# Performance work log

Measured on AMD Instinct MI355X. Metric: run time of the kernel, lower is better.

## Reference

```python
import jax, jax.numpy as jnp
import numpy as np

EPS = 1e-6

def setup_inputs() -> dict:
    key = jax.random.key(0)
    ks = jax.random.split(key, 5)
    B, C, H, W = 16, 512, 64, 64
    D = C // 8
    x = jax.random.normal(ks[0], (B, C, H, W), dtype=jnp.float32)
    Wq = jax.random.normal(ks[1], (D, C), dtype=jnp.float32) * (1.0 / np.sqrt(C))
    Wk = jax.random.normal(ks[2], (D, C), dtype=jnp.float32) * (1.0 / np.sqrt(C))
    Wv = jax.random.normal(ks[3], (C, C), dtype=jnp.float32) * (1.0 / np.sqrt(C))
    bq = jnp.zeros((D,), jnp.float32)
    bk = jnp.zeros((D,), jnp.float32)
    bv = jnp.zeros((C,), jnp.float32)
    gamma = jnp.ones((1,), jnp.float32)
    return {"x": x, "Wq": Wq, "bq": bq, "Wk": Wk, "bk": bk, "Wv": Wv, "bv": bv, "gamma": gamma}

def reference(x, Wq, bq, Wk, bk, Wv, bv, gamma):
    B, C, H, W = x.shape
    n = H * W
    xf = x.reshape(B, C, n)                                   # flatten spatial -> sequence
    # 1x1 convs == per-pixel linear projections
    Q = jnp.einsum('dc,bcn->bnd', Wq, xf) + bq                # (B, n, d)
    K = jnp.einsum('dc,bcn->bdn', Wk, xf) + bk[:, None]       # (B, d, n)
    V = jnp.einsum('dc,bcn->bdn', Wv, xf) + bv[:, None]       # (B, C, n)
    Q = jax.nn.softplus(Q)
    K = jax.nn.softplus(K)
    KV = jnp.einsum('bmn,bcn->bmc', K, V)                     # (B, d, C) linear-attention aggregation
    norm = 1.0 / jnp.einsum('bnm,bm->bn', Q, K.sum(-1) + EPS)  # (B, n)
    wv = jnp.einsum('bnm,bmc,bn->bcn', Q, KV, norm)           # (B, C, n)
    return (x + gamma[0] * wv.reshape(B, C, H, W))
```

## Files before the change

kernel.cpp:

```cpp
#include <hip/hip_runtime.h>
#include <hip/hip_bf16.h>
#include <math.h>

#define BB 16
#define CC 512
#define DD 64
#define NN 4096
#define EPSV 1e-6f
#define NCH 8

typedef __attribute__((ext_vector_type(8))) short short8;
typedef __attribute__((ext_vector_type(4))) short s16x4;
typedef __attribute__((ext_vector_type(4))) float f32x4;

__device__ __forceinline__ float softplus_f(float v) {
    return fmaxf(v, 0.0f) + __logf(1.0f + __expf(-fabsf(v)));
}
__device__ __forceinline__ short bf16s(float f) {
    __hip_bfloat16 h = __float2bfloat16(f);
    return __builtin_bit_cast(short, h);
}
__device__ __forceinline__ float sbf16(short s) {
    return __bfloat162float(__builtin_bit_cast(__hip_bfloat16, s));
}

__global__ __launch_bounds__(256) void k_prep(const float* __restrict__ Wq,
                                              const float* __restrict__ Wk,
                                              __hip_bfloat16* __restrict__ Wcat,
                                              float* __restrict__ Ksum) {
    int blk = blockIdx.x;
    if (blk < 256) {
        int i = blk * 256 + threadIdx.x;
        int j = i >> 9, c = i & 511;
        float v = (j < DD) ? Wq[j * CC + c] : Wk[(j - DD) * CC + c];
        Wcat[i] = __float2bfloat16(v);
    } else {
        f32x4 z = {0.f, 0.f, 0.f, 0.f};
        reinterpret_cast<f32x4*>(Ksum)[threadIdx.x] = z;
    }
}

__global__ __launch_bounds__(256) void k_proj(const float* __restrict__ x,
                                              const __hip_bfloat16* __restrict__ Wcat,
                                              const float* __restrict__ bq,
                                              const float* __restrict__ bk,
                                              __hip_bfloat16* __restrict__ Qb,
                                              __hip_bfloat16* __restrict__ Kb,
                                              __hip_bfloat16* __restrict__ xb16,
                                              float* __restrict__ Ksum) {
    __shared__ unsigned short xs[2][32][132];
    __shared__ unsigned short ws[2][128][40];

    int b = blockIdx.y;
    int n_blk = blockIdx.x * 128;
    int t = threadIdx.x;
    int wave = t >> 6, lane = t & 63;
    int nwl = wave * 32;
    int n_wave = n_blk + nwl;
    int l16 = lane & 15, g = lane >> 4;

    int sv = t & 31;
    int sc = t >> 5;
    int wj = t >> 1;
    int wh = t & 1;

    const float* xb = x + (size_t)b * CC * NN + n_blk + sv * 4;
    unsigned short* xg = reinterpret_cast<unsigned short*>(xb16)
                         + (size_t)b * CC * NN + n_blk + sv * 4;
    const unsigned short* wg = reinterpret_cast<const unsigned short*>(Wcat)
                               + (size_t)wj * 512 + wh * 16;

    f32x4 xr[4];
    s16x4 wr[4];

    auto loadx = [&](int c0) {
#pragma unroll
        for (int i = 0; i < 4; ++i)
            xr[i] = *reinterpret_cast<const f32x4*>(xb + (size_t)(c0 + sc + i * 8) * NN);
    };
    auto loadw = [&](int c0) {
#pragma unroll
        for (int k = 0; k < 4; ++k)
            wr[k] = *reinterpret_cast<const s16x4*>(wg + c0 + k * 4);
    };
    auto writex = [&](int bi, int c0) {
#pragma unroll
        for (int i = 0; i < 4; ++i) {
            s16x4 pv;
#pragma unroll
            for (int j = 0; j < 4; ++j) pv[j] = bf16s(xr[i][j]);
            *reinterpret_cast<s16x4*>(&xs[bi][sc + i * 8][sv * 4]) = pv;
            *reinterpret_cast<s16x4*>(&xg[(size_t)(c0 + sc + i * 8) * NN]) = pv;
        }
    };
    auto writew = [&](int bi) {
#pragma unroll
        for (int k = 0; k < 4; ++k)
            *reinterpret_cast<s16x4*>(&ws[bi][wj][wh * 16 + k * 4]) = wr[k];
    };

    f32x4 accQ[2][4] = {};
    f32x4 accK[4][2] = {};

    loadx(0); loadw(0);
    writex(0, 0); writew(0);

    for (int ck = 0; ck < 16; ++ck) {
        int cur = ck & 1;
        if (ck < 15) { loadx((ck + 1) * 32); loadw((ck + 1) * 32); }
        asm volatile("s_waitcnt lgkmcnt(0)" ::: "memory");
        __builtin_amdgcn_s_barrier();
        short8 xf[2], wf[8];
#pragma unroll
        for (int nf = 0; nf < 2; ++nf) {
            short8 v;
#pragma unroll
            for (int e = 0; e < 8; ++e)
                v[e] = (short)xs[cur][g * 8 + e][nwl + nf * 16 + l16];
            xf[nf] = v;
        }
#pragma unroll
        for (int jf = 0; jf < 8; ++jf)
            wf[jf] = *reinterpret_cast<const short8*>(&ws[cur][jf * 16 + l16][g * 8]);
#pragma unroll
        for (int nf = 0; nf < 2; ++nf)
#pragma unroll
            for (int jf = 0; jf < 4; ++jf)
                accQ[nf][jf] = __builtin_amdgcn_mfma_f32_16x16x32_bf16(xf[nf], wf[jf], accQ[nf][jf], 0, 0, 0);
#pragma unroll
        for (int jf = 0; jf < 4; ++jf)
#pragma unroll
            for (int nf = 0; nf < 2; ++nf)
                accK[jf][nf] = __builtin_amdgcn_mfma_f32_16x16x32_bf16(wf[4 + jf], xf[nf], accK[jf][nf], 0, 0, 0);
        if (ck < 15) { writex(cur ^ 1, (ck + 1) * 32); writew(cur ^ 1); }
    }

#pragma unroll
    for (int nf = 0; nf < 2; ++nf)
#pragma unroll
        for (int jf = 0; jf < 4; ++jf)
#pragma unroll
            for (int r = 0; r < 4; ++r) {
                int n = n_wave + nf * 16 + 4 * g + r;
                int j = jf * 16 + l16;
                float v = softplus_f(accQ[nf][jf][r] + bq[j]);
                Qb[((size_t)b * NN + n) * DD + j] = __float2bfloat16(v);
            }
#pragma unroll
    for (int jf = 0; jf < 4; ++jf)
#pragma unroll
        for (int r = 0; r < 4; ++r) {
            int m = jf * 16 + 4 * g + r;
            float s = 0.f;
#pragma unroll
            for (int nf = 0; nf < 2; ++nf) {
                int n = n_wave + nf * 16 + l16;
                float v = softplus_f(accK[jf][nf][r] + bk[m]);
                Kb[((size_t)b * DD + m) * NN + n] = __float2bfloat16(v);
                s += v;
            }
            s += __shfl_xor(s, 1, 64);
            s += __shfl_xor(s, 2, 64);
            s += __shfl_xor(s, 4, 64);
            s += __shfl_xor(s, 8, 64);
            if (l16 == 0) atomicAdd(&Ksum[b * DD + m], s);
        }
}

__global__ __launch_bounds__(256) void k_kx(const __hip_bfloat16* __restrict__ Kb,
                                            const __hip_bfloat16* __restrict__ xb16,
                                            float* __restrict__ KXp) {
    int b = blockIdx.z;
    int ch = blockIdx.y;
    int n0 = ch * 512;
    int c0 = blockIdx.x * 256;
    int wave = threadIdx.x >> 6, lane = threadIdx.x & 63;
    int cw = c0 + wave * 64;
    int l16 = lane & 15, g = lane >> 4;

    f32x4 acc[4][4] = {};
    const __hip_bfloat16* kp = Kb + (size_t)b * DD * NN;
    const __hip_bfloat16* xp = xb16 + (size_t)b * CC * NN;

#pragma unroll 4
    for (int ks = 0; ks < 16; ++ks) {
        int nk = n0 + ks * 32 + g * 8;
        short8 af[4], bf[4];
#pragma unroll
        for (int mi = 0; mi < 4; ++mi)
            af[mi] = *reinterpret_cast<const short8*>(kp + (size_t)(mi * 16 + l16) * NN + nk);
#pragma unroll
        for (int cj = 0; cj < 4; ++cj)
            bf[cj] = *reinterpret_cast<const short8*>(xp + (size_t)(cw + cj * 16 + l16) * NN + nk);
#pragma unroll
        for (int mi = 0; mi < 4; ++mi)
#pragma unroll
            for (int cj = 0; cj < 4; ++cj)
                acc[mi][cj] = __builtin_amdgcn_mfma_f32_16x16x32_bf16(af[mi], bf[cj], acc[mi][cj], 0, 0, 0);
    }
    float* kxd = KXp + (size_t)ch * BB * DD * CC + (size_t)b * DD * CC;
#pragma unroll
    for (int mi = 0; mi < 4; ++mi)
#pragma unroll
        for (int cj = 0; cj < 4; ++cj)
#pragma unroll
            for (int r = 0; r < 4; ++r) {
                int m = mi * 16 + 4 * g + r;
                int c = cw + cj * 16 + l16;
                kxd[(size_t)m * CC + c] = acc[mi][cj][r];
            }
}

__global__ __launch_bounds__(256) void k_red(const float* __restrict__ KXp,
                                             float* __restrict__ KX) {
    size_t i = (size_t)blockIdx.x * 256 + threadIdx.x;
    const f32x4* src = reinterpret_cast<const f32x4*>(KXp);
    size_t chstride = (size_t)BB * DD * CC / 4;
    f32x4 s = src[i];
#pragma unroll
    for (int ch = 1; ch < NCH; ++ch) {
        f32x4 v = src[ch * chstride + i];
        s[0] += v[0]; s[1] += v[1]; s[2] += v[2]; s[3] += v[3];
    }
    reinterpret_cast<f32x4*>(KX)[i] = s;
}

__global__ __launch_bounds__(256) void k_kv(const float* __restrict__ KX,
                                            const float* __restrict__ Wv,
                                            const float* __restrict__ bv,
                                            const float* __restrict__ Ksum,
                                            __hip_bfloat16* __restrict__ KVTb) {
    int b = blockIdx.y;
    int c0 = blockIdx.x * 64;
    int wave = threadIdx.x >> 6, lane = threadIdx.x & 63;
    int cw = c0 + wave * 16;
    int l16 = lane & 15, g = lane >> 4;

    f32x4 acc[4] = {};
    const float* wvp = Wv + (size_t)(cw + l16) * CC;
    const float* kxp = KX + (size_t)b * DD * CC;

#pragma unroll
    for (int ck = 0; ck < 16; ++ck) {
        int cp = ck * 32 + g * 8;
        f32x4 w0 = *reinterpret_cast<const f32x4*>(wvp + cp);
        f32x4 w1 = *reinterpret_cast<const f32x4*>(wvp + cp + 4);
        short8 a_hi, a_lo;
#pragma unroll
        for (int e = 0; e < 4; ++e) {
            a_hi[e] = bf16s(w0[e]);     a_lo[e] = bf16s(w0[e] - sbf16(a_hi[e]));
            a_hi[4 + e] = bf16s(w1[e]); a_lo[4 + e] = bf16s(w1[e] - sbf16(a_hi[4 + e]));
        }
#pragma unroll
        for (int mj = 0; mj < 4; ++mj) {
            const float* kr = kxp + (size_t)(mj * 16 + l16) * CC + cp;
            f32x4 k0 = *reinterpret_cast<const f32x4*>(kr);
            f32x4 k1 = *reinterpret_cast<const f32x4*>(kr + 4);
            short8 b_hi, b_lo;
#pragma unroll
            for (int e = 0; e < 4; ++e) {
                b_hi[e] = bf16s(k0[e]);     b_lo[e] = bf16s(k0[e] - sbf16(b_hi[e]));
                b_hi[4 + e] = bf16s(k1[e]); b_lo[4 + e] = bf16s(k1[e] - sbf16(b_hi[4 + e]));
            }
            acc[mj] = __builtin_amdgcn_mfma_f32_16x16x32_bf16(a_hi, b_hi, acc[mj], 0, 0, 0);
            acc[mj] = __builtin_amdgcn_mfma_f32_16x16x32_bf16(a_lo, b_hi, acc[mj], 0, 0, 0);
            acc[mj] = __builtin_amdgcn_mfma_f32_16x16x32_bf16(a_hi, b_lo, acc[mj], 0, 0, 0);
        }
    }
#pragma unroll
    for (int mj = 0; mj < 4; ++mj)
#pragma unroll
        for (int r = 0; r < 4; ++r) {
            int c = cw + 4 * g + r;
            int m = mj * 16 + l16;
            KVTb[((size_t)b * CC + c) * DD + m] =
                __float2bfloat16(acc[mj][r] + bv[c] * Ksum[b * DD + m]);
        }
}

__global__ __launch_bounds__(256) void k_out(const __hip_bfloat16* __restrict__ xb16,
                                             const __hip_bfloat16* __restrict__ Qb,
                                             const __hip_bfloat16* __restrict__ KVTb,
                                             const float* __restrict__ Ksum,
                                             const float* __restrict__ gamma,
                                             float* __restrict__ out) {
    int b = blockIdx.z;
    int c_blk = blockIdx.x * 128, n_blk = blockIdx.y * 128;
    int wave = threadIdx.x >> 6, lane = threadIdx.x & 63;
    int cw = c_blk + (wave >> 1) * 64, nw = n_blk + (wave & 1) * 64;
    int l16 = lane & 15, g = lane >> 4;

    float ksv[2][8];
#pragma unroll
    for (int ck = 0; ck < 2; ++ck)
#pragma unroll
        for (int e = 0; e < 8; ++e)
            ksv[ck][e] = Ksum[b * DD + (ck * 4 + g) * 8 + e] + EPSV;

    f32x4 acc[4][4] = {};
    float dot[4] = {0.f, 0.f, 0.f, 0.f};
    const short8* ap = reinterpret_cast<const short8*>(KVTb) + ((size_t)b * CC + cw) * 8;
    const short8* bp = reinterpret_cast<const short8*>(Qb) + ((size_t)b * NN + nw) * 8;
#pragma unroll
    for (int ck = 0; ck < 2; ++ck) {
        int ch = ck * 4 + g;
        short8 af[4], bf[4];
#pragma unroll
        for (int i = 0; i < 4; ++i) af[i] = ap[(size_t)(i * 16 + l16) * 8 + ch];
#pragma unroll
        for (int i = 0; i < 4; ++i) bf[i] = bp[(size_t)(i * 16 + l16) * 8 + ch];
#pragma unroll
        for (int j = 0; j < 4; ++j)
#pragma unroll
            for (int e = 0; e < 8; ++e)
                dot[j] = fmaf(sbf16(bf[j][e]), ksv[ck][e], dot[j]);
#pragma unroll
        for (int i = 0; i < 4; ++i)
#pragma unroll
            for (int j = 0; j < 4; ++j)
                acc[i][j] = __builtin_amdgcn_mfma_f32_16x16x32_bf16(af[i], bf[j], acc[i][j], 0, 0, 0);
    }
    float gm = gamma[0];
    float sc[4];
#pragma unroll
    for (int j = 0; j < 4; ++j) {
        float d = dot[j];
        d += __shfl_xor(d, 16, 64);
        d += __shfl_xor(d, 32, 64);
        sc[j] = gm / d;
    }
    const __hip_bfloat16* xb = xb16 + (size_t)b * CC * NN;
    float* ob = out + (size_t)b * CC * NN;
#pragma unroll
    for (int i = 0; i < 4; ++i)
#pragma unroll
        for (int r = 0; r < 4; ++r) {
            int c = cw + i * 16 + 4 * g + r;
            size_t rowoff = (size_t)c * NN;
#pragma unroll
            for (int j = 0; j < 4; ++j) {
                int n = nw + j * 16 + l16;
                float xv = __bfloat162float(xb[rowoff + n]);
                __builtin_nontemporal_store(xv + sc[j] * acc[i][j][r], &ob[rowoff + n]);
            }
        }
}

extern "C" void kernel_launch(void* const* d_in, const int* in_sizes, int n_in,
                              void* d_out, int out_size, void* d_ws, size_t ws_size,
                              hipStream_t stream) {
    const float* x     = (const float*)d_in[0];
    const float* Wq    = (const float*)d_in[1];
    const float* bq    = (const float*)d_in[2];
    const float* Wk    = (const float*)d_in[3];
    const float* bk    = (const float*)d_in[4];
    const float* Wv    = (const float*)d_in[5];
    const float* bv    = (const float*)d_in[6];
    const float* gamma = (const float*)d_in[7];
    float* out = (float*)d_out;

    float* ws    = (float*)d_ws;
    float* KX    = ws;
    float* KXp   = KX + (size_t)BB * DD * CC;
    float* Ksum  = KXp + (size_t)NCH * BB * DD * CC;
    __hip_bfloat16* Qb   = (__hip_bfloat16*)(Ksum + BB * DD);
    __hip_bfloat16* Kb   = Qb + (size_t)BB * NN * DD;
    __hip_bfloat16* KVTb = Kb + (size_t)BB * DD * NN;
    __hip_bfloat16* Wcat = KVTb + (size_t)BB * CC * DD;
    __hip_bfloat16* xb16 = Wcat + 128 * CC;

    k_prep<<<dim3(257), dim3(256), 0, stream>>>(Wq, Wk, Wcat, Ksum);
    k_proj<<<dim3(NN / 128, BB), dim3(256), 0, stream>>>(x, Wcat, bq, bk, Qb, Kb, xb16, Ksum);
    k_kx<<<dim3(2, NCH, BB), dim3(256), 0, stream>>>(Kb, xb16, KXp);
    k_red<<<dim3(BB * DD * CC / 4 / 256), dim3(256), 0, stream>>>(KXp, KX);
    k_kv<<<dim3(CC / 64, BB), dim3(256), 0, stream>>>(KX, Wv, bv, Ksum, KVTb);
    k_out<<<dim3(CC / 128, NN / 128, BB), dim3(256), 0, stream>>>(xb16, Qb, KVTb, Ksum, gamma, out);
}
```

Measured before the change: 161.7 us.

## Store KX partials in bf16, drop split-bf16 MFMA, remap k_out block order

The K·x partial sums and their reduction are now stored in bf16 instead of fp32, which halves the traffic through the partial buffer. The KV product now runs a single bf16 MFMA in place of the three-pass hi/lo split. k_out switches to a 1D grid with a swizzled block-to-tile mapping that interleaves batches across block IDs, likely aimed at XCD or cache locality. Accuracy drops because the partials, the reduced KX and Wv are all rounded to bf16.

```diff
diff --git a/kernel.cpp b/kernel.cpp
--- a/kernel.cpp
+++ b/kernel.cpp
@@ -169,7 +169,7 @@
 
 __global__ __launch_bounds__(256) void k_kx(const __hip_bfloat16* __restrict__ Kb,
                                             const __hip_bfloat16* __restrict__ xb16,
-                                            float* __restrict__ KXp) {
+                                            unsigned short* __restrict__ KXpb) {
     int b = blockIdx.z;
     int ch = blockIdx.y;
     int n0 = ch * 512;
@@ -198,7 +198,7 @@
             for (int cj = 0; cj < 4; ++cj)
                 acc[mi][cj] = __builtin_amdgcn_mfma_f32_16x16x32_bf16(af[mi], bf[cj], acc[mi][cj], 0, 0, 0);
     }
-    float* kxd = KXp + (size_t)ch * BB * DD * CC + (size_t)b * DD * CC;
+    unsigned short* kxd = KXpb + (size_t)ch * BB * DD * CC + (size_t)b * DD * CC;
 #pragma unroll
     for (int mi = 0; mi < 4; ++mi)
 #pragma unroll
@@ -207,25 +207,29 @@
             for (int r = 0; r < 4; ++r) {
                 int m = mi * 16 + 4 * g + r;
                 int c = cw + cj * 16 + l16;
-                kxd[(size_t)m * CC + c] = acc[mi][cj][r];
+                kxd[(size_t)m * CC + c] = (unsigned short)bf16s(acc[mi][cj][r]);
             }
 }
 
-__global__ __launch_bounds__(256) void k_red(const float* __restrict__ KXp,
-                                             float* __restrict__ KX) {
+__global__ __launch_bounds__(256) void k_red(const unsigned short* __restrict__ KXpb,
+                                             unsigned short* __restrict__ KXb) {
     size_t i = (size_t)blockIdx.x * 256 + threadIdx.x;
-    const f32x4* src = reinterpret_cast<const f32x4*>(KXp);
-    size_t chstride = (size_t)BB * DD * CC / 4;
-    f32x4 s = src[i];
-#pragma unroll
-    for (int ch = 1; ch < NCH; ++ch) {
-        f32x4 v = src[ch * chstride + i];
-        s[0] += v[0]; s[1] += v[1]; s[2] += v[2]; s[3] += v[3];
-    }
-    reinterpret_cast<f32x4*>(KX)[i] = s;
-}
-
-__global__ __launch_bounds__(256) void k_kv(const float* __restrict__ KX,
+    const short8* src = reinterpret_cast<const short8*>(KXpb);
+    size_t chstride = (size_t)BB * DD * CC / 8;
+    float s[8] = {};
+#pragma unroll
+    for (int ch = 0; ch < NCH; ++ch) {
+        short8 v = src[ch * chstride + i];
+#pragma unroll
+        for (int e = 0; e < 8; ++e) s[e] += sbf16(v[e]);
+    }
+    short8 o;
+#pragma unroll
+    for (int e = 0; e < 8; ++e) o[e] = bf16s(s[e]);
+    reinterpret_cast<short8*>(KXb)[i] = o;
+}
+
+__global__ __launch_bounds__(256) void k_kv(const unsigned short* __restrict__ KXb,
                                             const float* __restrict__ Wv,
                                             const float* __restrict__ bv,
                                             const float* __restrict__ Ksum,
@@ -238,33 +242,20 @@
 
     f32x4 acc[4] = {};
     const float* wvp = Wv + (size_t)(cw + l16) * CC;
-    const float* kxp = KX + (size_t)b * DD * CC;
+    const unsigned short* kxp = KXb + (size_t)b * DD * CC;
 
 #pragma unroll
     for (int ck = 0; ck < 16; ++ck) {
         int cp = ck * 32 + g * 8;
         f32x4 w0 = *reinterpret_cast<const f32x4*>(wvp + cp);
         f32x4 w1 = *reinterpret_cast<const f32x4*>(wvp + cp + 4);
-        short8 a_hi, a_lo;
-#pragma unroll
-        for (int e = 0; e < 4; ++e) {
-            a_hi[e] = bf16s(w0[e]);     a_lo[e] = bf16s(w0[e] - sbf16(a_hi[e]));
-            a_hi[4 + e] = bf16s(w1[e]); a_lo[4 + e] = bf16s(w1[e] - sbf16(a_hi[4 + e]));
-        }
+        short8 a;
+#pragma unroll
+        for (int e = 0; e < 4; ++e) { a[e] = bf16s(w0[e]); a[4 + e] = bf16s(w1[e]); }
 #pragma unroll
         for (int mj = 0; mj < 4; ++mj) {
-            const float* kr = kxp + (size_t)(mj * 16 + l16) * CC + cp;
-            f32x4 k0 = *reinterpret_cast<const f32x4*>(kr);
-            f32x4 k1 = *reinterpret_cast<const f32x4*>(kr + 4);
-            short8 b_hi, b_lo;
-#pragma unroll
-            for (int e = 0; e < 4; ++e) {
-                b_hi[e] = bf16s(k0[e]);     b_lo[e] = bf16s(k0[e] - sbf16(b_hi[e]));
-                b_hi[4 + e] = bf16s(k1[e]); b_lo[4 + e] = bf16s(k1[e] - sbf16(b_hi[4 + e]));
-            }
-            acc[mj] = __builtin_amdgcn_mfma_f32_16x16x32_bf16(a_hi, b_hi, acc[mj], 0, 0, 0);
-            acc[mj] = __builtin_amdgcn_mfma_f32_16x16x32_bf16(a_lo, b_hi, acc[mj], 0, 0, 0);
-            acc[mj] = __builtin_amdgcn_mfma_f32_16x16x32_bf16(a_hi, b_lo, acc[mj], 0, 0, 0);
+            short8 bfr = *reinterpret_cast<const short8*>(kxp + (size_t)(mj * 16 + l16) * CC + cp);
+            acc[mj] = __builtin_amdgcn_mfma_f32_16x16x32_bf16(a, bfr, acc[mj], 0, 0, 0);
         }
     }
 #pragma unroll
@@ -284,8 +275,12 @@
                                              const float* __restrict__ Ksum,
                                              const float* __restrict__ gamma,
                                              float* __restrict__ out) {
-    int b = blockIdx.z;
-    int c_blk = blockIdx.x * 128, n_blk = blockIdx.y * 128;
+    int d = blockIdx.x;
+    int logical = (d & 7) * 256 + (d >> 3);
+    int c_blk = (logical & 3) * 128;
+    int n_blk = ((logical >> 2) & 31) * 128;
+    int b = logical >> 7;
+
     int wave = threadIdx.x >> 6, lane = threadIdx.x & 63;
     int cw = c_blk + (wave >> 1) * 64, nw = n_blk + (wave & 1) * 64;
     int l16 = lane & 15, g = lane >> 4;
@@ -324,10 +319,10 @@
     float sc[4];
 #pragma unroll
     for (int j = 0; j < 4; ++j) {
-        float d = dot[j];
-        d += __shfl_xor(d, 16, 64);
-        d += __shfl_xor(d, 32, 64);
-        sc[j] = gm / d;
+        float d2 = dot[j];
+        d2 += __shfl_xor(d2, 16, 64);
+        d2 += __shfl_xor(d2, 32, 64);
+        sc[j] = gm / d2;
     }
     const __hip_bfloat16* xb = xb16 + (size_t)b * CC * NN;
     float* ob = out + (size_t)b * CC * NN;
@@ -360,9 +355,9 @@
     float* out = (float*)d_out;
 
     float* ws    = (float*)d_ws;
-    float* KX    = ws;
-    float* KXp   = KX + (size_t)BB * DD * CC;
-    float* Ksum  = KXp + (size_t)NCH * BB * DD * CC;
+    unsigned short* KXb  = (unsigned short*)ws;
+    unsigned short* KXpb = KXb + (size_t)BB * DD * CC;
+    float* Ksum  = (float*)(KXpb + (size_t)NCH * BB * DD * CC);
     __hip_bfloat16* Qb   = (__hip_bfloat16*)(Ksum + BB * DD);
     __hip_bfloat16* Kb   = Qb + (size_t)BB * NN * DD;
     __hip_bfloat16* KVTb = Kb + (size_t)BB * DD * NN;
@@ -371,8 +366,8 @@
 
     k_prep<<<dim3(257), dim3(256), 0, stream>>>(Wq, Wk, Wcat, Ksum);
     k_proj<<<dim3(NN / 128, BB), dim3(256), 0, stream>>>(x, Wcat, bq, bk, Qb, Kb, xb16, Ksum);
-    k_kx<<<dim3(2, NCH, BB), dim3(256), 0, stream>>>(Kb, xb16, KXp);
-    k_red<<<dim3(BB * DD * CC / 4 / 256), dim3(256), 0, stream>>>(KXp, KX);
-    k_kv<<<dim3(CC / 64, BB), dim3(256), 0, stream>>>(KX, Wv, bv, Ksum, KVTb);
-    k_out<<<dim3(CC / 128, NN / 128, BB), dim3(256), 0, stream>>>(xb16, Qb, KVTb, Ksum, gamma, out);
-}
+    k_kx<<<dim3(2, NCH, BB), dim3(256), 0, stream>>>(Kb, xb16, KXpb);
+    k_red<<<dim3(BB * DD * CC / 8 / 256), dim3(256), 0, stream>>>(KXpb, KXb);
+    k_kv<<<dim3(CC / 64, BB), dim3(256), 0, stream>>>(KXb, Wv, bv, Ksum, KVTb);
+    k_out<<<dim3(2048), dim3(256), 0, stream>>>(xb16, Qb, KVTb, Ksum, gamma, out);
+}
```

New measurement: 146.5 us, median of 2. -9.4%, faster.
